# Kernel tuning notes

Measured on AMD Instinct MI355X. Metric: run time of the kernel, lower is better.

## Reference

```python
import jax, jax.numpy as jnp
import numpy as np

N = 100000      # nodes
E = 3200000     # edges (before self-loops)
F_IN = 512      # input feature dim
H1, H2 = 64, 128
C = 40          # num classes
EPS = 1e-5      # BatchNorm eps


def setup_inputs() -> dict:
    key = jax.random.key(0)
    ks = jax.random.split(key, 20)
    inp = {
        "x": jax.random.normal(ks[0], (N, F_IN), jnp.float32),
        "edge_index": jax.random.randint(ks[1], (2, E), 0, N, dtype=jnp.int64),
        # GCNConv weights/biases (glorot-ish scale)
        "W1": jax.random.normal(ks[2], (F_IN, H1), jnp.float32) * (1.0 / np.sqrt(F_IN)),
        "b1": jnp.zeros((H1,), jnp.float32),
        "W2": jax.random.normal(ks[3], (H1, H2), jnp.float32) * (1.0 / np.sqrt(H1)),
        "b2": jnp.zeros((H2,), jnp.float32),
        "W3": jax.random.normal(ks[4], (H2, C), jnp.float32) * (1.0 / np.sqrt(H2)),
        "b3": jnp.zeros((C,), jnp.float32),
        # BatchNorm (eval mode: running stats)
        "g1": 1.0 + 0.1 * jax.random.normal(ks[5], (H1,), jnp.float32),
        "bt1": 0.1 * jax.random.normal(ks[6], (H1,), jnp.float32),
        "rm1": 0.1 * jax.random.normal(ks[7], (H1,), jnp.float32),
        "rv1": jax.random.uniform(ks[8], (H1,), jnp.float32, 0.5, 1.5),
        "g2": 1.0 + 0.1 * jax.random.normal(ks[9], (H2,), jnp.float32),
        "bt2": 0.1 * jax.random.normal(ks[10], (H2,), jnp.float32),
        "rm2": 0.1 * jax.random.normal(ks[11], (H2,), jnp.float32),
        "rv2": jax.random.uniform(ks[12], (H2,), jnp.float32, 0.5, 1.5),
    }
    return inp


def _gcn_norm(edge_index):
    # add self-loops, compute sym-normalized edge weights: d^-1/2[src]*d^-1/2[dst]
    loop = jnp.arange(N, dtype=edge_index.dtype)
    src = jnp.concatenate([edge_index[0], loop])
    dst = jnp.concatenate([edge_index[1], loop])
    deg = jax.ops.segment_sum(jnp.ones_like(dst, jnp.float32), dst, num_segments=N)
    dinv = 1.0 / jnp.sqrt(deg)  # deg >= 1 thanks to self-loops
    norm = dinv[src] * dinv[dst]  # [E+N]
    return src, dst, norm


def _gcn_conv(x, W, b, src, dst, norm):
    h = x @ W                                   # [N, out]
    msg = h[src] * norm[:, None]                # [E+N, out] gather + per-edge scale
    agg = jax.ops.segment_sum(msg, dst, num_segments=N)  # scatter-add
    return agg + b


def _bn_eval(x, gamma, beta, mean, var):
    return (x - mean) * (gamma / jnp.sqrt(var + EPS)) + beta


def reference(x, edge_index, W1, b1, W2, b2, W3, b3,
              g1, bt1, rm1, rv1, g2, bt2, rm2, rv2):
    src, dst, norm = _gcn_norm(edge_index)
    h = jax.nn.relu(_bn_eval(_gcn_conv(x, W1, b1, src, dst, norm), g1, bt1, rm1, rv1))
    # dropout p=0.3: identity in eval mode
    h = jax.nn.relu(_bn_eval(_gcn_conv(h, W2, b2, src, dst, norm), g2, bt2, rm2, rv2))
    h = _gcn_conv(h, W3, b3, src, dst, norm)
    return jax.nn.log_softmax(h, axis=1)
```

## Files before the change

### kernel.cpp

```cpp
#include <hip/hip_runtime.h>
#include <hip/hip_bf16.h>

#define NN 100000
#define FIN 512
#define H1D 64
#define H2D 128
#define CD 40
#define GP 64
#define BNEPS 1e-5f

#define BSHIFT 9
#define BSZ 512
#define NB 196
#define CHUNK 8192

typedef __attribute__((ext_vector_type(8))) short bf16x8;
typedef __attribute__((ext_vector_type(4))) float f32x4;

__device__ __forceinline__ float bf2f(ushort u) {
    union { uint i; float f; } v; v.i = ((uint)u) << 16; return v.f;
}
__device__ __forceinline__ ushort f2bf(float f) {
    union { float f; uint i; } v; v.f = f;
    uint x = v.i;
    return (ushort)((x + 0x7fffu + ((x >> 16) & 1u)) >> 16);
}

__device__ __forceinline__ void acc8(float* a, uint4 v) {
    a[0] += bf2f((ushort)(v.x & 0xffff)); a[1] += bf2f((ushort)(v.x >> 16));
    a[2] += bf2f((ushort)(v.y & 0xffff)); a[3] += bf2f((ushort)(v.y >> 16));
    a[4] += bf2f((ushort)(v.z & 0xffff)); a[5] += bf2f((ushort)(v.z >> 16));
    a[6] += bf2f((ushort)(v.w & 0xffff)); a[7] += bf2f((ushort)(v.w >> 16));
}

__device__ __forceinline__ uint4 selz(bool q, uint4 v) {
    return q ? v : make_uint4(0u, 0u, 0u, 0u);
}


__global__ __launch_bounds__(256) void bhist_k(const int* __restrict__ dst, int E,
                                               int* __restrict__ bcount) {
    __shared__ int h[NB];
    for (int i = threadIdx.x; i < NB; i += 256) h[i] = 0;
    __syncthreads();
    int i = blockIdx.x * blockDim.x + threadIdx.x;
    int st = gridDim.x * blockDim.x;
    for (; i < E; i += st) atomicAdd(&h[dst[i] >> BSHIFT], 1);
    __syncthreads();
    for (int j = threadIdx.x; j < NB; j += 256)
        if (h[j]) atomicAdd(&bcount[j], h[j]);
}

__global__ __launch_bounds__(256) void bscan_k(const int* __restrict__ bcount,
                                               int* __restrict__ bstart,
                                               int* __restrict__ bcursor) {
    __shared__ int sh[NB];
    int tid = threadIdx.x;
    if (tid < NB) sh[tid] = bcount[tid];
    __syncthreads();
    for (int off = 1; off < NB; off <<= 1) {
        int v = (tid < NB && tid >= off) ? sh[tid - off] : 0;
        __syncthreads();
        if (tid < NB) sh[tid] += v;
        __syncthreads();
    }
    if (tid < NB) {
        int s = tid ? sh[tid - 1] : 0;
        bstart[tid] = s;
        bcursor[tid] = s;
    }
    if (tid == 0) bstart[NB] = sh[NB - 1];
}

__global__ __launch_bounds__(256) void bscatter_k(const int* __restrict__ src,
                                                  const int* __restrict__ dst, int E,
                                                  int* __restrict__ bcursor,
                                                  int* __restrict__ ebuf) {
    __shared__ int hist[NB];
    __shared__ int loff[NB];
    __shared__ int lcur[NB];
    __shared__ int gbase[NB];
    __shared__ int sbuf[CHUNK];
    int tid = threadIdx.x;
    int e0 = blockIdx.x * CHUNK;
    int e1 = e0 + CHUNK; if (e1 > E) e1 = E;

    for (int i = tid; i < NB; i += 256) hist[i] = 0;
    __syncthreads();
    for (int i = e0 + tid; i < e1; i += 256) atomicAdd(&hist[dst[i] >> BSHIFT], 1);
    __syncthreads();
    int v = (tid < NB) ? hist[tid] : 0;
    __syncthreads();
    if (tid < NB) loff[tid] = v;
    __syncthreads();
    for (int off = 1; off < NB; off <<= 1) {
        int u = (tid < NB && tid >= off) ? loff[tid - off] : 0;
        __syncthreads();
        if (tid < NB) loff[tid] += u;
        __syncthreads();
    }
    if (tid < NB) {
        int excl = loff[tid] - v;
        loff[tid] = excl;
        lcur[tid] = excl;
        gbase[tid] = (v > 0) ? atomicAdd(&bcursor[tid], v) : 0;
    }
    __syncthreads();
    for (int i = e0 + tid; i < e1; i += 256) {
        int d = dst[i];
        int b = d >> BSHIFT;
        int pos = atomicAdd(&lcur[b], 1);
        sbuf[pos] = (src[i] << BSHIFT) | (d & (BSZ - 1));
    }
    __syncthreads();
    int wave = tid >> 6, lane = tid & 63;
    for (int b = wave; b < NB; b += 4) {
        int cnt = (b + 1 < NB ? loff[b + 1] : (e1 - e0)) - loff[b];
        int s0 = loff[b], d0 = gbase[b];
        for (int k = lane; k < cnt; k += 64) ebuf[d0 + k] = sbuf[s0 + k];
    }
}

__global__ __launch_bounds__(256) void bcsr_k(const int* __restrict__ ebuf,
                                              const int* __restrict__ bstart,
                                              int* __restrict__ rowstart,
                                              float* __restrict__ dinv,
                                              int* __restrict__ csr, int E) {
    __shared__ int ldeg[BSZ];
    __shared__ int lcur[BSZ];
    __shared__ int s2[256];
    int b = blockIdx.x, tid = threadIdx.x;
    int node0 = b << BSHIFT;
    int es = bstart[b], ee = bstart[b + 1];
    ldeg[tid] = 0; ldeg[tid + 256] = 0;
    __syncthreads();
    for (int i = es + tid; i < ee; i += 256) atomicAdd(&ldeg[ebuf[i] & (BSZ - 1)], 1);
    __syncthreads();
    int a0 = ldeg[2 * tid], a1 = ldeg[2 * tid + 1];
    s2[tid] = a0 + a1;
    __syncthreads();
    for (int off = 1; off < 256; off <<= 1) {
        int u = (tid >= off) ? s2[tid - off] : 0;
        __syncthreads();
        s2[tid] += u;
        __syncthreads();
    }
    int base2 = tid ? s2[tid - 1] : 0;
    int ex0 = base2, ex1 = base2 + a0;
    int n0 = node0 + 2 * tid, n1 = n0 + 1;
    if (n0 < NN) { rowstart[n0] = es + ex0; dinv[n0] = rsqrtf((float)(a0 + 1)); }
    if (n1 < NN) { rowstart[n1] = es + ex1; dinv[n1] = rsqrtf((float)(a1 + 1)); }
    lcur[2 * tid] = es + ex0;
    lcur[2 * tid + 1] = es + ex1;
    __syncthreads();
    for (int i = es + tid; i < ee; i += 256) {
        int e = ebuf[i];
        int pos = atomicAdd(&lcur[e & (BSZ - 1)], 1);
        csr[pos] = ((unsigned)e) >> BSHIFT;
    }
    if (b == 0 && tid == 0) rowstart[NN] = E;
}

__global__ __launch_bounds__(256) void w1cvt_k(const float* __restrict__ W1,
                                               ushort* __restrict__ w1t) {
    int i = blockIdx.x * 256 + threadIdx.x;
    if (i < FIN * H1D) {
        int n = i >> 9, k = i & 511;
        w1t[i] = f2bf(W1[k * H1D + n]);
    }
}

#define BPAD 520
__global__ __launch_bounds__(256) void gemm1_k(const float* __restrict__ x,
                                               const ushort* __restrict__ w1t,
                                               const float* __restrict__ dinv,
                                               ushort* __restrict__ t1) {
    __shared__ ushort sB[H1D * BPAD];
    int tid = threadIdx.x;
    {
        int row = tid >> 2, seg = tid & 3;
        const uint4* srcp = (const uint4*)(w1t + row * FIN + seg * 128);
        uint4* dstp = (uint4*)(sB + row * BPAD + seg * 128);
#pragma unroll
        for (int j = 0; j < 16; ++j) dstp[j] = srcp[j];
    }
    __syncthreads();
    int wave = tid >> 6, lane = tid & 63;
    int lm = lane & 15, q = lane >> 4;
    int r0 = blockIdx.x * 64 + wave * 16;
    int mrow = r0 + lm;
    int mc = mrow < NN ? mrow : NN - 1;
    const float* ap = x + (size_t)mc * FIN + q * 8;
    const ushort* bp = sB + (size_t)lm * BPAD + q * 8;
    f32x4 acc0 = {0.f, 0.f, 0.f, 0.f}, acc1 = acc0, acc2 = acc0, acc3 = acc0;
#pragma unroll 4
    for (int kb = 0; kb < FIN; kb += 32) {
        f32x4 a01 = __builtin_nontemporal_load((const f32x4*)(ap + kb));
        f32x4 a23 = __builtin_nontemporal_load((const f32x4*)(ap + kb + 4));
        union { bf16x8 v8; __hip_bfloat162 h2[4]; } ua;
        ua.h2[0] = __float22bfloat162_rn(make_float2(a01[0], a01[1]));
        ua.h2[1] = __float22bfloat162_rn(make_float2(a01[2], a01[3]));
        ua.h2[2] = __float22bfloat162_rn(make_float2(a23[0], a23[1]));
        ua.h2[3] = __float22bfloat162_rn(make_float2(a23[2], a23[3]));
        bf16x8 b0 = *(const bf16x8*)(bp + kb);
        bf16x8 b1 = *(const bf16x8*)(bp + 16 * BPAD + kb);
        bf16x8 b2 = *(const bf16x8*)(bp + 32 * BPAD + kb);
        bf16x8 b3 = *(const bf16x8*)(bp + 48 * BPAD + kb);
        acc0 = __builtin_amdgcn_mfma_f32_16x16x32_bf16(ua.v8, b0, acc0, 0, 0, 0);
        acc1 = __builtin_amdgcn_mfma_f32_16x16x32_bf16(ua.v8, b1, acc1, 0, 0, 0);
        acc2 = __builtin_amdgcn_mfma_f32_16x16x32_bf16(ua.v8, b2, acc2, 0, 0, 0);
        acc3 = __builtin_amdgcn_mfma_f32_16x16x32_bf16(ua.v8, b3, acc3, 0, 0, 0);
    }
    int rbase = r0 + q * 4;
#pragma unroll
    for (int r = 0; r < 4; ++r) {
        int row = rbase + r;
        if (row < NN) {
            float dv = dinv[row];
            ushort* o = t1 + (size_t)row * H1D;
            o[lm]      = f2bf(acc0[r] * dv);
            o[16 + lm] = f2bf(acc1[r] * dv);
            o[32 + lm] = f2bf(acc2[r] * dv);
            o[48 + lm] = f2bf(acc3[r] * dv);
        }
    }
}

template <int MODE>
__global__ __launch_bounds__(256) void agg64_k(const ushort* __restrict__ tin,
                                               ushort* __restrict__ tout,
                                               const int* __restrict__ rowstart,
                                               const int* __restrict__ csr,
                                               const float* __restrict__ dinv,
                                               const float* __restrict__ g,
                                               const float* __restrict__ bt,
                                               const float* __restrict__ rm,
                                               const float* __restrict__ rv,
                                               const float* __restrict__ b,
                                               int E) {
    int w = (blockIdx.x * blockDim.x + threadIdx.x) >> 6;
    int lane = threadIdx.x & 63;
    int nA = 2 * w;
    if (nA >= NN) return;
    int nB = nA + 1;
    int gsl = lane >> 3, c = lane & 7;
    int base = 8 * c;
    int2 r01 = *(const int2*)(rowstart + nA);
    int reB = rowstart[nA + 2];
    int iA = r01.x, reA = r01.y;
    int iB = reA;
    int Em1 = E - 1;
    float a[8], y[8];
#pragma unroll
    for (int j = 0; j < 8; ++j) { a[j] = 0.f; y[j] = 0.f; }

    for (;;) {
        bool dA = (iA + 32 <= reA);
        bool dB = (iB + 32 <= reB);
        if (!(dA | dB)) break;
        int jA0 = dA ? iA + gsl      : Em1;
        int jA1 = dA ? iA + 8 + gsl  : Em1;
        int jA2 = dA ? iA + 16 + gsl : Em1;
        int jA3 = dA ? iA + 24 + gsl : Em1;
        int jB0 = dB ? iB + gsl      : Em1;
        int jB1 = dB ? iB + 8 + gsl  : Em1;
        int jB2 = dB ? iB + 16 + gsl : Em1;
        int jB3 = dB ? iB + 24 + gsl : Em1;
        int sA0 = csr[jA0], sA1 = csr[jA1], sA2 = csr[jA2], sA3 = csr[jA3];
        int sB0 = csr[jB0], sB1 = csr[jB1], sB2 = csr[jB2], sB3 = csr[jB3];
        uint4 vA0 = *(const uint4*)(tin + (size_t)sA0 * H1D + base);
        uint4 vA1 = *(const uint4*)(tin + (size_t)sA1 * H1D + base);
        uint4 vA2 = *(const uint4*)(tin + (size_t)sA2 * H1D + base);
        uint4 vA3 = *(const uint4*)(tin + (size_t)sA3 * H1D + base);
        uint4 vB0 = *(const uint4*)(tin + (size_t)sB0 * H1D + base);
        uint4 vB1 = *(const uint4*)(tin + (size_t)sB1 * H1D + base);
        uint4 vB2 = *(const uint4*)(tin + (size_t)sB2 * H1D + base);
        uint4 vB3 = *(const uint4*)(tin + (size_t)sB3 * H1D + base);
        vA0 = selz(dA, vA0); vA1 = selz(dA, vA1); vA2 = selz(dA, vA2); vA3 = selz(dA, vA3);
        vB0 = selz(dB, vB0); vB1 = selz(dB, vB1); vB2 = selz(dB, vB2); vB3 = selz(dB, vB3);
        acc8(a, vA0); acc8(a, vA1); acc8(a, vA2); acc8(a, vA3);
        acc8(y, vB0); acc8(y, vB1); acc8(y, vB2); acc8(y, vB3);
        iA += dA ? 32 : 0;
        iB += dB ? 32 : 0;
    }
    {
        bool qA0 = iA + gsl < reA,      qB0 = iB + gsl < reB;
        bool qA1 = iA + 8 + gsl < reA,  qB1 = iB + 8 + gsl < reB;
        bool qA2 = iA + 16 + gsl < reA, qB2 = iB + 16 + gsl < reB;
        bool qA3 = iA + 24 + gsl < reA, qB3 = iB + 24 + gsl < reB;
        int jA0 = qA0 ? iA + gsl      : Em1;
        int jA1 = qA1 ? iA + 8 + gsl  : Em1;
        int jA2 = qA2 ? iA + 16 + gsl : Em1;
        int jA3 = qA3 ? iA + 24 + gsl : Em1;
        int jB0 = qB0 ? iB + gsl      : Em1;
        int jB1 = qB1 ? iB + 8 + gsl  : Em1;
        int jB2 = qB2 ? iB + 16 + gsl : Em1;
        int jB3 = qB3 ? iB + 24 + gsl : Em1;
        int sA0 = csr[jA0], sA1 = csr[jA1], sA2 = csr[jA2], sA3 = csr[jA3];
        int sB0 = csr[jB0], sB1 = csr[jB1], sB2 = csr[jB2], sB3 = csr[jB3];
        uint4 vA0 = *(const uint4*)(tin + (size_t)sA0 * H1D + base);
        uint4 vA1 = *(const uint4*)(tin + (size_t)sA1 * H1D + base);
        uint4 vA2 = *(const uint4*)(tin + (size_t)sA2 * H1D + base);
        uint4 vA3 = *(const uint4*)(tin + (size_t)sA3 * H1D + base);
        uint4 vB0 = *(const uint4*)(tin + (size_t)sB0 * H1D + base);
        uint4 vB1 = *(const uint4*)(tin + (size_t)sB1 * H1D + base);
        uint4 vB2 = *(const uint4*)(tin + (size_t)sB2 * H1D + base);
        uint4 vB3 = *(const uint4*)(tin + (size_t)sB3 * H1D + base);
        vA0 = selz(qA0, vA0); vA1 = selz(qA1, vA1); vA2 = selz(qA2, vA2); vA3 = selz(qA3, vA3);
        vB0 = selz(qB0, vB0); vB1 = selz(qB1, vB1); vB2 = selz(qB2, vB2); vB3 = selz(qB3, vB3);
        acc8(a, vA0); acc8(a, vA1); acc8(a, vA2); acc8(a, vA3);
        acc8(y, vB0); acc8(y, vB1); acc8(y, vB2); acc8(y, vB3);
    }
    uint4 svA = *(const uint4*)(tin + (size_t)nA * H1D + base);
    uint4 svB = *(const uint4*)(tin + (size_t)nB * H1D + base);
#pragma unroll
    for (int j = 0; j < 8; ++j) a[j] += __shfl_xor(a[j], 8);
#pragma unroll
    for (int j = 0; j < 8; ++j) a[j] += __shfl_xor(a[j], 16);
#pragma unroll
    for (int j = 0; j < 8; ++j) a[j] += __shfl_xor(a[j], 32);
#pragma unroll
    for (int j = 0; j < 8; ++j) y[j] += __shfl_xor(y[j], 8);
#pragma unroll
    for (int j = 0; j < 8; ++j) y[j] += __shfl_xor(y[j], 16);
#pragma unroll
    for (int j = 0; j < 8; ++j) y[j] += __shfl_xor(y[j], 32);
    acc8(a, svA);
    acc8(y, svB);
    float2 dv2 = *(const float2*)(dinv + nA);
    float dv = (gsl == 0) ? dv2.x : dv2.y;
    float s[8];
#pragma unroll
    for (int j = 0; j < 8; ++j) s[j] = (gsl == 0) ? a[j] : y[j];
    float z[8];
    if (MODE == 1) {
        int f0 = base;
        float4 G0 = *(const float4*)(g + f0),  G1 = *(const float4*)(g + f0 + 4);
        float4 V0 = *(const float4*)(rv + f0), V1 = *(const float4*)(rv + f0 + 4);
        float4 B0 = *(const float4*)(b + f0),  B1 = *(const float4*)(b + f0 + 4);
        float4 M0 = *(const float4*)(rm + f0), M1 = *(const float4*)(rm + f0 + 4);
        float4 T0 = *(const float4*)(bt + f0), T1 = *(const float4*)(bt + f0 + 4);
        float sc[8] = { G0.x * rsqrtf(V0.x + BNEPS), G0.y * rsqrtf(V0.y + BNEPS),
                        G0.z * rsqrtf(V0.z + BNEPS), G0.w * rsqrtf(V0.w + BNEPS),
                        G1.x * rsqrtf(V1.x + BNEPS), G1.y * rsqrtf(V1.y + BNEPS),
                        G1.z * rsqrtf(V1.z + BNEPS), G1.w * rsqrtf(V1.w + BNEPS) };
        float sh[8] = { (B0.x - M0.x) * sc[0] + T0.x, (B0.y - M0.y) * sc[1] + T0.y,
                        (B0.z - M0.z) * sc[2] + T0.z, (B0.w - M0.w) * sc[3] + T0.w,
                        (B1.x - M1.x) * sc[4] + T1.x, (B1.y - M1.y) * sc[5] + T1.y,
                        (B1.z - M1.z) * sc[6] + T1.z, (B1.w - M1.w) * sc[7] + T1.w };
#pragma unroll
        for (int j = 0; j < 8; ++j)
            z[j] = fmaxf(s[j] * dv * sc[j] + sh[j], 0.f) * dv;
    } else {
#pragma unroll
        for (int j = 0; j < 8; ++j) z[j] = s[j] * dv;
    }
    if (gsl < 2) {
        uint4 o;
        o.x = (uint)f2bf(z[0]) | ((uint)f2bf(z[1]) << 16);
        o.y = (uint)f2bf(z[2]) | ((uint)f2bf(z[3]) << 16);
        o.z = (uint)f2bf(z[4]) | ((uint)f2bf(z[5]) << 16);
        o.w = (uint)f2bf(z[6]) | ((uint)f2bf(z[7]) << 16);
        *(uint4*)(tout + (size_t)(nA + gsl) * H1D + base) = o;
    }
}

__global__ __launch_bounds__(256) void p2p3_k(const ushort* __restrict__ u2,
                                              const float* __restrict__ W2,
                                              const float* __restrict__ b2,
                                              const float* __restrict__ W3,
                                              const float* __restrict__ g2,
                                              const float* __restrict__ bt2,
                                              const float* __restrict__ rm2,
                                              const float* __restrict__ rv2,
                                              const float* __restrict__ dinv,
                                              ushort* __restrict__ g3) {
    __shared__ float sW2[H1D * H2D];
    __shared__ float sW3[H2D * CD];
    __shared__ float sc2[H2D], sh2[H2D];
    int tid = threadIdx.x;
    for (int i = tid; i < H1D * H2D; i += 256) sW2[i] = W2[i];
    for (int i = tid; i < H2D * CD; i += 256) sW3[i] = W3[i];
    if (tid < H2D) {
        float s = g2[tid] * rsqrtf(rv2[tid] + BNEPS);
        sc2[tid] = s;
        sh2[tid] = (b2[tid] - rm2[tid]) * s + bt2[tid];
    }
    __syncthreads();
    int node = blockIdx.x * 256 + tid;
    if (node >= NN) return;
    float u[H1D];
    const uint4* up = (const uint4*)(u2 + (size_t)node * H1D);
#pragma unroll
    for (int i = 0; i < 8; ++i) {
        uint4 v = up[i];
        u[8 * i + 0] = bf2f((ushort)(v.x & 0xffff)); u[8 * i + 1] = bf2f((ushort)(v.x >> 16));
        u[8 * i + 2] = bf2f((ushort)(v.y & 0xffff)); u[8 * i + 3] = bf2f((ushort)(v.y >> 16));
        u[8 * i + 4] = bf2f((ushort)(v.z & 0xffff)); u[8 * i + 5] = bf2f((ushort)(v.z >> 16));
        u[8 * i + 6] = bf2f((ushort)(v.w & 0xffff)); u[8 * i + 7] = bf2f((ushort)(v.w >> 16));
    }
    float gacc[CD];
#pragma unroll
    for (int c = 0; c < CD; ++c) gacc[c] = 0.f;
    for (int fc = 0; fc < H2D; fc += 32) {
        float a[32];
#pragma unroll
        for (int j = 0; j < 32; ++j) a[j] = 0.f;
        for (int l = 0; l < H1D; ++l) {
            float ul = u[l];
            const float4* wr = (const float4*)&sW2[l * H2D + fc];
#pragma unroll
            for (int j = 0; j < 8; ++j) {
                float4 w = wr[j];
                a[4 * j]     += ul * w.x;
                a[4 * j + 1] += ul * w.y;
                a[4 * j + 2] += ul * w.z;
                a[4 * j + 3] += ul * w.w;
            }
        }
#pragma unroll
        for (int j = 0; j < 32; ++j) {
            int f = fc + j;
            float hv = fmaxf(a[j] * sc2[f] + sh2[f], 0.f);
            const float4* w3r = (const float4*)&sW3[f * CD];
#pragma unroll
            for (int c = 0; c < 10; ++c) {
                float4 w = w3r[c];
                gacc[4 * c]     += hv * w.x;
                gacc[4 * c + 1] += hv * w.y;
                gacc[4 * c + 2] += hv * w.z;
                gacc[4 * c + 3] += hv * w.w;
            }
        }
    }
    float dv = dinv[node];
    ushort* op = g3 + (size_t)node * GP;
#pragma unroll
    for (int c = 0; c < 10; ++c) {
        uint pk  = (uint)f2bf(gacc[4 * c] * dv)     | ((uint)f2bf(gacc[4 * c + 1] * dv) << 16);
        uint pk2 = (uint)f2bf(gacc[4 * c + 2] * dv) | ((uint)f2bf(gacc[4 * c + 3] * dv) << 16);
        *(uint2*)&op[4 * c] = make_uint2(pk, pk2);
    }
}

__global__ __launch_bounds__(256) void agg40_k(const ushort* __restrict__ g3,
                                               const float* __restrict__ b3,
                                               const int* __restrict__ rowstart,
                                               const int* __restrict__ csr,
                                               const float* __restrict__ dinv,
                                               float* __restrict__ out,
                                               int E) {
    int w = (blockIdx.x * blockDim.x + threadIdx.x) >> 6;
    int lane = threadIdx.x & 63;
    int nA = 2 * w;
    if (nA >= NN) return;
    int nB = nA + 1;
    int gsl = lane >> 3, c = lane & 7;
    int base = 8 * c;
    int2 r01 = *(const int2*)(rowstart + nA);
    int reB = rowstart[nA + 2];
    int iA = r01.x, reA = r01.y;
    int iB = reA;
    int Em1 = E - 1;
    float a[8], y[8];
#pragma unroll
    for (int j = 0; j < 8; ++j) { a[j] = 0.f; y[j] = 0.f; }

    for (;;) {
        bool dA = (iA + 32 <= reA);
        bool dB = (iB + 32 <= reB);
        if (!(dA | dB)) break;
        int jA0 = dA ? iA + gsl      : Em1;
        int jA1 = dA ? iA + 8 + gsl  : Em1;
        int jA2 = dA ? iA + 16 + gsl : Em1;
        int jA3 = dA ? iA + 24 + gsl : Em1;
        int jB0 = dB ? iB + gsl      : Em1;
        int jB1 = dB ? iB + 8 + gsl  : Em1;
        int jB2 = dB ? iB + 16 + gsl : Em1;
        int jB3 = dB ? iB + 24 + gsl : Em1;
        int sA0 = csr[jA0], sA1 = csr[jA1], sA2 = csr[jA2], sA3 = csr[jA3];
        int sB0 = csr[jB0], sB1 = csr[jB1], sB2 = csr[jB2], sB3 = csr[jB3];
        uint4 vA0 = *(const uint4*)(g3 + (size_t)sA0 * GP + base);
        uint4 vA1 = *(const uint4*)(g3 + (size_t)sA1 * GP + base);
        uint4 vA2 = *(const uint4*)(g3 + (size_t)sA2 * GP + base);
        uint4 vA3 = *(const uint4*)(g3 + (size_t)sA3 * GP + base);
        uint4 vB0 = *(const uint4*)(g3 + (size_t)sB0 * GP + base);
        uint4 vB1 = *(const uint4*)(g3 + (size_t)sB1 * GP + base);
        uint4 vB2 = *(const uint4*)(g3 + (size_t)sB2 * GP + base);
        uint4 vB3 = *(const uint4*)(g3 + (size_t)sB3 * GP + base);
        vA0 = selz(dA, vA0); vA1 = selz(dA, vA1); vA2 = selz(dA, vA2); vA3 = selz(dA, vA3);
        vB0 = selz(dB, vB0); vB1 = selz(dB, vB1); vB2 = selz(dB, vB2); vB3 = selz(dB, vB3);
        acc8(a, vA0); acc8(a, vA1); acc8(a, vA2); acc8(a, vA3);
        acc8(y, vB0); acc8(y, vB1); acc8(y, vB2); acc8(y, vB3);
        iA += dA ? 32 : 0;
        iB += dB ? 32 : 0;
    }
    {
        bool qA0 = iA + gsl < reA,      qB0 = iB + gsl < reB;
        bool qA1 = iA + 8 + gsl < reA,  qB1 = iB + 8 + gsl < reB;
        bool qA2 = iA + 16 + gsl < reA, qB2 = iB + 16 + gsl < reB;
        bool qA3 = iA + 24 + gsl < reA, qB3 = iB + 24 + gsl < reB;
        int jA0 = qA0 ? iA + gsl      : Em1;
        int jA1 = qA1 ? iA + 8 + gsl  : Em1;
        int jA2 = qA2 ? iA + 16 + gsl : Em1;
        int jA3 = qA3 ? iA + 24 + gsl : Em1;
        int jB0 = qB0 ? iB + gsl      : Em1;
        int jB1 = qB1 ? iB + 8 + gsl  : Em1;
        int jB2 = qB2 ? iB + 16 + gsl : Em1;
        int jB3 = qB3 ? iB + 24 + gsl : Em1;
        int sA0 = csr[jA0], sA1 = csr[jA1], sA2 = csr[jA2], sA3 = csr[jA3];
        int sB0 = csr[jB0], sB1 = csr[jB1], sB2 = csr[jB2], sB3 = csr[jB3];
        uint4 vA0 = *(const uint4*)(g3 + (size_t)sA0 * GP + base);
        uint4 vA1 = *(const uint4*)(g3 + (size_t)sA1 * GP + base);
        uint4 vA2 = *(const uint4*)(g3 + (size_t)sA2 * GP + base);
        uint4 vA3 = *(const uint4*)(g3 + (size_t)sA3 * GP + base);
        uint4 vB0 = *(const uint4*)(g3 + (size_t)sB0 * GP + base);
        uint4 vB1 = *(const uint4*)(g3 + (size_t)sB1 * GP + base);
        uint4 vB2 = *(const uint4*)(g3 + (size_t)sB2 * GP + base);
        uint4 vB3 = *(const uint4*)(g3 + (size_t)sB3 * GP + base);
        vA0 = selz(qA0, vA0); vA1 = selz(qA1, vA1); vA2 = selz(qA2, vA2); vA3 = selz(qA3, vA3);
        vB0 = selz(qB0, vB0); vB1 = selz(qB1, vB1); vB2 = selz(qB2, vB2); vB3 = selz(qB3, vB3);
        acc8(a, vA0); acc8(a, vA1); acc8(a, vA2); acc8(a, vA3);
        acc8(y, vB0); acc8(y, vB1); acc8(y, vB2); acc8(y, vB3);
    }
    uint4 svA = *(const uint4*)(g3 + (size_t)nA * GP + base);
    uint4 svB = *(const uint4*)(g3 + (size_t)nB * GP + base);
#pragma unroll
    for (int j = 0; j < 8; ++j) a[j] += __shfl_xor(a[j], 8);
#pragma unroll
    for (int j = 0; j < 8; ++j) a[j] += __shfl_xor(a[j], 16);
#pragma unroll
    for (int j = 0; j < 8; ++j) a[j] += __shfl_xor(a[j], 32);
#pragma unroll
    for (int j = 0; j < 8; ++j) y[j] += __shfl_xor(y[j], 8);
#pragma unroll
    for (int j = 0; j < 8; ++j) y[j] += __shfl_xor(y[j], 16);
#pragma unroll
    for (int j = 0; j < 8; ++j) y[j] += __shfl_xor(y[j], 32);
    acc8(a, svA);
    acc8(y, svB);
    float2 dv2 = *(const float2*)(dinv + nA);
    float dv = (gsl == 0) ? dv2.x : dv2.y;
    float s[8];
#pragma unroll
    for (int j = 0; j < 8; ++j) s[j] = (gsl == 0) ? a[j] : y[j];
    float z[8];
    if (c < 5) {
        float4 bb0 = *(const float4*)(b3 + base);
        float4 bb1 = *(const float4*)(b3 + base + 4);
        z[0] = s[0] * dv + bb0.x; z[1] = s[1] * dv + bb0.y;
        z[2] = s[2] * dv + bb0.z; z[3] = s[3] * dv + bb0.w;
        z[4] = s[4] * dv + bb1.x; z[5] = s[5] * dv + bb1.y;
        z[6] = s[6] * dv + bb1.z; z[7] = s[7] * dv + bb1.w;
    } else {
#pragma unroll
        for (int j = 0; j < 8; ++j) z[j] = -1e30f;
    }
    float m = fmaxf(fmaxf(fmaxf(z[0], z[1]), fmaxf(z[2], z[3])),
                    fmaxf(fmaxf(z[4], z[5]), fmaxf(z[6], z[7])));
    m = fmaxf(m, __shfl_xor(m, 1));
    m = fmaxf(m, __shfl_xor(m, 2));
    m = fmaxf(m, __shfl_xor(m, 4));
    float e = 0.f;
    if (c < 5) {
#pragma unroll
        for (int j = 0; j < 8; ++j) e += __expf(z[j] - m);
    }
    e += __shfl_xor(e, 1);
    e += __shfl_xor(e, 2);
    e += __shfl_xor(e, 4);
    float ls = __logf(e);
    if (gsl < 2 && c < 5) {
        float4 o0 = { z[0] - m - ls, z[1] - m - ls, z[2] - m - ls, z[3] - m - ls };
        float4 o1 = { z[4] - m - ls, z[5] - m - ls, z[6] - m - ls, z[7] - m - ls };
        float* orow = out + (size_t)(nA + gsl) * CD + base;
        *(float4*)(orow)     = o0;
        *(float4*)(orow + 4) = o1;
    }
}


extern "C" void kernel_launch(void* const* d_in, const int* in_sizes, int n_in,
                              void* d_out, int out_size, void* d_ws, size_t ws_size,
                              hipStream_t stream) {
    (void)n_in; (void)out_size; (void)ws_size;
    const float* x   = (const float*)d_in[0];
    const int*   ei  = (const int*)d_in[1];
    const float* W1  = (const float*)d_in[2];
    const float* b1  = (const float*)d_in[3];
    const float* W2  = (const float*)d_in[4];
    const float* b2  = (const float*)d_in[5];
    const float* W3  = (const float*)d_in[6];
    const float* b3  = (const float*)d_in[7];
    const float* g1  = (const float*)d_in[8];
    const float* bt1 = (const float*)d_in[9];
    const float* rm1 = (const float*)d_in[10];
    const float* rv1 = (const float*)d_in[11];
    const float* g2  = (const float*)d_in[12];
    const float* bt2 = (const float*)d_in[13];
    const float* rm2 = (const float*)d_in[14];
    const float* rv2 = (const float*)d_in[15];
    float* out = (float*)d_out;
    const int E = in_sizes[1] / 2;

    char* w = (char*)d_ws;
    auto alloc = [&](size_t bytes) { char* p = w; w += (bytes + 511) & ~(size_t)511; return p; };
    int*    bcount   = (int*)alloc((size_t)NB * 4);
    int*    bstart   = (int*)alloc((size_t)(NB + 1) * 4);
    int*    bcursor  = (int*)alloc((size_t)NB * 4);
    int*    rowstart = (int*)alloc((size_t)(NN + 1) * 4);
    float*  dinv     = (float*)alloc((size_t)NN * 4);
    int*    csr      = (int*)alloc((size_t)E * 4);
    int*    ebuf     = (int*)alloc((size_t)E * 4);
    ushort* w1t      = (ushort*)alloc((size_t)H1D * FIN * 2);
    ushort* t1       = (ushort*)alloc((size_t)NN * H1D * 2);
    ushort* t2       = (ushort*)alloc((size_t)NN * H1D * 2);
    ushort* g3       = (ushort*)alloc((size_t)NN * GP * 2);

    const int aggblocks = ((NN / 2) + 3) / 4;

    hipMemsetAsync(bcount, 0, (size_t)NB * 4, stream);
    bhist_k<<<512, 256, 0, stream>>>(ei + E, E, bcount);
    bscan_k<<<1, 256, 0, stream>>>(bcount, bstart, bcursor);
    bscatter_k<<<(E + CHUNK - 1) / CHUNK, 256, 0, stream>>>(ei, ei + E, E, bcursor, ebuf);
    bcsr_k<<<NB, 256, 0, stream>>>(ebuf, bstart, rowstart, dinv, csr, E);
    w1cvt_k<<<(FIN * H1D + 255) / 256, 256, 0, stream>>>(W1, w1t);
    gemm1_k<<<(NN + 63) / 64, 256, 0, stream>>>(x, w1t, dinv, t1);
    agg64_k<1><<<aggblocks, 256, 0, stream>>>(t1, t2, rowstart, csr, dinv, g1, bt1, rm1, rv1, b1, E);
    agg64_k<2><<<aggblocks, 256, 0, stream>>>(t2, t1, rowstart, csr, dinv, nullptr, nullptr, nullptr, nullptr, nullptr, E);
    p2p3_k<<<(NN + 255) / 256, 256, 0, stream>>>(t1, W2, b2, W3, g2, bt2, rm2, rv2, dinv, g3);
    agg40_k<<<aggblocks, 256, 0, stream>>>(g3, b3, rowstart, csr, dinv, out, E);
}
```

Before: 714.0 us.

## Fuse second aggregation with W2/W3 projection; enlarge gemm1 blocks to 512 threads

Replaces the separate layer-2 aggregation kernel and per-node dense projection kernel with one kernel. It aggregates neighbours per wave, stages the aggregated rows in shared memory, then does the W2 (bf16-packed) and W3 (transposed) matvecs cooperatively across lanes. This removes a full intermediate write and read of the N×64 tensor and one launch. It also replaces the register-heavy per-thread matvec, at the cost of bf16 rounding of W2. Separately, gemm1 now uses 512-thread blocks covering 128 rows each, so the W1 tile staged in shared memory is shared by twice as many rows.

After: 756.2 us. 5.9% more time.

```diff
diff --git a/kernel.cpp b/kernel.cpp
--- a/kernel.cpp
+++ b/kernel.cpp
@@ -171,23 +171,23 @@
 }
 
 #define BPAD 520
-__global__ __launch_bounds__(256) void gemm1_k(const float* __restrict__ x,
+__global__ __launch_bounds__(512) void gemm1_k(const float* __restrict__ x,
                                                const ushort* __restrict__ w1t,
                                                const float* __restrict__ dinv,
                                                ushort* __restrict__ t1) {
     __shared__ ushort sB[H1D * BPAD];
     int tid = threadIdx.x;
     {
-        int row = tid >> 2, seg = tid & 3;
-        const uint4* srcp = (const uint4*)(w1t + row * FIN + seg * 128);
-        uint4* dstp = (uint4*)(sB + row * BPAD + seg * 128);
-#pragma unroll
-        for (int j = 0; j < 16; ++j) dstp[j] = srcp[j];
+        int row = tid >> 3, seg = tid & 7;
+        const uint4* srcp = (const uint4*)(w1t + row * FIN + seg * 64);
+        uint4* dstp = (uint4*)(sB + row * BPAD + seg * 64);
+#pragma unroll
+        for (int j = 0; j < 8; ++j) dstp[j] = srcp[j];
     }
     __syncthreads();
     int wave = tid >> 6, lane = tid & 63;
     int lm = lane & 15, q = lane >> 4;
-    int r0 = blockIdx.x * 64 + wave * 16;
+    int r0 = blockIdx.x * 128 + wave * 16;
     int mrow = r0 + lm;
     int mc = mrow < NN ? mrow : NN - 1;
     const float* ap = x + (size_t)mc * FIN + q * 8;
@@ -365,7 +365,8 @@
     }
 }
 
-__global__ __launch_bounds__(256) void p2p3_k(const ushort* __restrict__ u2,
+#define APB 8
+__global__ __launch_bounds__(256) void aggp_k(const ushort* __restrict__ tin,
                                               const float* __restrict__ W2,
                                               const float* __restrict__ b2,
                                               const float* __restrict__ W3,
@@ -373,73 +374,168 @@
                                               const float* __restrict__ bt2,
                                               const float* __restrict__ rm2,
                                               const float* __restrict__ rv2,
+                                              const int* __restrict__ rowstart,
+                                              const int* __restrict__ csr,
                                               const float* __restrict__ dinv,
-                                              ushort* __restrict__ g3) {
-    __shared__ float sW2[H1D * H2D];
-    __shared__ float sW3[H2D * CD];
+                                              ushort* __restrict__ g3,
+                                              int E) {
+    __shared__ uint  sW2p[H1D * 64];
+    __shared__ float sW3T[CD][132];
     __shared__ float sc2[H2D], sh2[H2D];
+    __shared__ float su[APB][H1D];
+    __shared__ float sh[APB][H2D];
     int tid = threadIdx.x;
-    for (int i = tid; i < H1D * H2D; i += 256) sW2[i] = W2[i];
-    for (int i = tid; i < H2D * CD; i += 256) sW3[i] = W3[i];
+    for (int i = tid; i < H1D * 64; i += 256) {
+        int l = i >> 6, fl = i & 63;
+        uint pk = (uint)f2bf(W2[l * H2D + fl]) | ((uint)f2bf(W2[l * H2D + 64 + fl]) << 16);
+        sW2p[i] = pk;
+    }
+    for (int i = tid; i < H2D * CD; i += 256) {
+        int f = i / CD, o = i - f * CD;
+        sW3T[o][f] = W3[i];
+    }
     if (tid < H2D) {
         float s = g2[tid] * rsqrtf(rv2[tid] + BNEPS);
         sc2[tid] = s;
         sh2[tid] = (b2[tid] - rm2[tid]) * s + bt2[tid];
     }
     __syncthreads();
-    int node = blockIdx.x * 256 + tid;
-    if (node >= NN) return;
-    float u[H1D];
-    const uint4* up = (const uint4*)(u2 + (size_t)node * H1D);
-#pragma unroll
-    for (int i = 0; i < 8; ++i) {
-        uint4 v = up[i];
-        u[8 * i + 0] = bf2f((ushort)(v.x & 0xffff)); u[8 * i + 1] = bf2f((ushort)(v.x >> 16));
-        u[8 * i + 2] = bf2f((ushort)(v.y & 0xffff)); u[8 * i + 3] = bf2f((ushort)(v.y >> 16));
-        u[8 * i + 4] = bf2f((ushort)(v.z & 0xffff)); u[8 * i + 5] = bf2f((ushort)(v.z >> 16));
-        u[8 * i + 6] = bf2f((ushort)(v.w & 0xffff)); u[8 * i + 7] = bf2f((ushort)(v.w >> 16));
-    }
-    float gacc[CD];
-#pragma unroll
-    for (int c = 0; c < CD; ++c) gacc[c] = 0.f;
-    for (int fc = 0; fc < H2D; fc += 32) {
-        float a[32];
-#pragma unroll
-        for (int j = 0; j < 32; ++j) a[j] = 0.f;
-        for (int l = 0; l < H1D; ++l) {
-            float ul = u[l];
-            const float4* wr = (const float4*)&sW2[l * H2D + fc];
-#pragma unroll
-            for (int j = 0; j < 8; ++j) {
-                float4 w = wr[j];
-                a[4 * j]     += ul * w.x;
-                a[4 * j + 1] += ul * w.y;
-                a[4 * j + 2] += ul * w.z;
-                a[4 * j + 3] += ul * w.w;
-            }
+    int wave = tid >> 6, lane = tid & 63;
+    int nA = blockIdx.x * APB + 2 * wave;
+    if (nA >= NN) return;
+    int nB = nA + 1;
+    int gsl = lane >> 3, c = lane & 7;
+    int base = 8 * c;
+    int2 r01 = *(const int2*)(rowstart + nA);
+    int reB = rowstart[nA + 2];
+    int iA = r01.x, reA = r01.y;
+    int iB = reA;
+    int Em1 = E - 1;
+    float a[8], y[8];
+#pragma unroll
+    for (int j = 0; j < 8; ++j) { a[j] = 0.f; y[j] = 0.f; }
+
+    for (;;) {
+        bool dA = (iA + 32 <= reA);
+        bool dB = (iB + 32 <= reB);
+        if (!(dA | dB)) break;
+        int jA0 = dA ? iA + gsl      : Em1;
+        int jA1 = dA ? iA + 8 + gsl  : Em1;
+        int jA2 = dA ? iA + 16 + gsl : Em1;
+        int jA3 = dA ? iA + 24 + gsl : Em1;
+        int jB0 = dB ? iB + gsl      : Em1;
+        int jB1 = dB ? iB + 8 + gsl  : Em1;
+        int jB2 = dB ? iB + 16 + gsl : Em1;
+        int jB3 = dB ? iB + 24 + gsl : Em1;
+        int sA0 = csr[jA0], sA1 = csr[jA1], sA2 = csr[jA2], sA3 = csr[jA3];
+        int sB0 = csr[jB0], sB1 = csr[jB1], sB2 = csr[jB2], sB3 = csr[jB3];
+        uint4 vA0 = *(const uint4*)(tin + (size_t)sA0 * H1D + base);
+        uint4 vA1 = *(const uint4*)(tin + (size_t)sA1 * H1D + base);
+        uint4 vA2 = *(const uint4*)(tin + (size_t)sA2 * H1D + base);
+        uint4 vA3 = *(const uint4*)(tin + (size_t)sA3 * H1D + base);
+        uint4 vB0 = *(const uint4*)(tin + (size_t)sB0 * H1D + base);
+        uint4 vB1 = *(const uint4*)(tin + (size_t)sB1 * H1D + base);
+        uint4 vB2 = *(const uint4*)(tin + (size_t)sB2 * H1D + base);
+        uint4 vB3 = *(const uint4*)(tin + (size_t)sB3 * H1D + base);
+        vA0 = selz(dA, vA0); vA1 = selz(dA, vA1); vA2 = selz(dA, vA2); vA3 = selz(dA, vA3);
+        vB0 = selz(dB, vB0); vB1 = selz(dB, vB1); vB2 = selz(dB, vB2); vB3 = selz(dB, vB3);
+        acc8(a, vA0); acc8(a, vA1); acc8(a, vA2); acc8(a, vA3);
+        acc8(y, vB0); acc8(y, vB1); acc8(y, vB2); acc8(y, vB3);
+        iA += dA ? 32 : 0;
+        iB += dB ? 32 : 0;
+    }
+    {
+        bool qA0 = iA + gsl < reA,      qB0 = iB + gsl < reB;
+        bool qA1 = iA + 8 + gsl < reA,  qB1 = iB + 8 + gsl < reB;
+        bool qA2 = iA + 16 + gsl < reA, qB2 = iB + 16 + gsl < reB;
+        bool qA3 = iA + 24 + gsl < reA, qB3 = iB + 24 + gsl < reB;
+        int jA0 = qA0 ? iA + gsl      : Em1;
+        int jA1 = qA1 ? iA + 8 + gsl  : Em1;
+        int jA2 = qA2 ? iA + 16 + gsl : Em1;
+        int jA3 = qA3 ? iA + 24 + gsl : Em1;
+        int jB0 = qB0 ? iB + gsl      : Em1;
+        int jB1 = qB1 ? iB + 8 + gsl  : Em1;
+        int jB2 = qB2 ? iB + 16 + gsl : Em1;
+        int jB3 = qB3 ? iB + 24 + gsl : Em1;
+        int sA0 = csr[jA0], sA1 = csr[jA1], sA2 = csr[jA2], sA3 = csr[jA3];
+        int sB0 = csr[jB0], sB1 = csr[jB1], sB2 = csr[jB2], sB3 = csr[jB3];
+        uint4 vA0 = *(const uint4*)(tin + (size_t)sA0 * H1D + base);
+        uint4 vA1 = *(const uint4*)(tin + (size_t)sA1 * H1D + base);
+        uint4 vA2 = *(const uint4*)(tin + (size_t)sA2 * H1D + base);
+        uint4 vA3 = *(const uint4*)(tin + (size_t)sA3 * H1D + base);
+        uint4 vB0 = *(const uint4*)(tin + (size_t)sB0 * H1D + base);
+        uint4 vB1 = *(const uint4*)(tin + (size_t)sB1 * H1D + base);
+        uint4 vB2 = *(const uint4*)(tin + (size_t)sB2 * H1D + base);
+        uint4 vB3 = *(const uint4*)(tin + (size_t)sB3 * H1D + base);
+        vA0 = selz(qA0, vA0); vA1 = selz(qA1, vA1); vA2 = selz(qA2, vA2); vA3 = selz(qA3, vA3);
+        vB0 = selz(qB0, vB0); vB1 = selz(qB1, vB1); vB2 = selz(qB2, vB2); vB3 = selz(qB3, vB3);
+        acc8(a, vA0); acc8(a, vA1); acc8(a, vA2); acc8(a, vA3);
+        acc8(y, vB0); acc8(y, vB1); acc8(y, vB2); acc8(y, vB3);
+    }
+    uint4 svA = *(const uint4*)(tin + (size_t)nA * H1D + base);
+    uint4 svB = *(const uint4*)(tin + (size_t)nB * H1D + base);
+#pragma unroll
+    for (int j = 0; j < 8; ++j) a[j] += __shfl_xor(a[j], 8);
+#pragma unroll
+    for (int j = 0; j < 8; ++j) a[j] += __shfl_xor(a[j], 16);
+#pragma unroll
+    for (int j = 0; j < 8; ++j) a[j] += __shfl_xor(a[j], 32);
+#pragma unroll
+    for (int j = 0; j < 8; ++j) y[j] += __shfl_xor(y[j], 8);
+#pragma unroll
+    for (int j = 0; j < 8; ++j) y[j] += __shfl_xor(y[j], 16);
+#pragma unroll
+    for (int j = 0; j < 8; ++j) y[j] += __shfl_xor(y[j], 32);
+    acc8(a, svA);
+    acc8(y, svB);
+    float2 dv2 = *(const float2*)(dinv + nA);
+    if (gsl < 2) {
+        float dv = (gsl == 0) ? dv2.x : dv2.y;
+        int n = 2 * wave + gsl;
+        float s0 = (gsl == 0) ? a[0] : y[0], s1 = (gsl == 0) ? a[1] : y[1];
+        float s2v = (gsl == 0) ? a[2] : y[2], s3 = (gsl == 0) ? a[3] : y[3];
+        float s4 = (gsl == 0) ? a[4] : y[4], s5 = (gsl == 0) ? a[5] : y[5];
+        float s6 = (gsl == 0) ? a[6] : y[6], s7 = (gsl == 0) ? a[7] : y[7];
+        *(float4*)&su[n][base]     = make_float4(s0 * dv, s1 * dv, s2v * dv, s3 * dv);
+        *(float4*)&su[n][base + 4] = make_float4(s4 * dv, s5 * dv, s6 * dv, s7 * dv);
+    }
+    int n0 = 2 * wave, n1 = n0 + 1;
+    float hA0 = 0.f, hA1 = 0.f, hB0 = 0.f, hB1 = 0.f;
+#pragma unroll 4
+    for (int l4 = 0; l4 < H1D / 4; ++l4) {
+        float4 uA4 = *(const float4*)&su[n0][4 * l4];
+        float4 uB4 = *(const float4*)&su[n1][4 * l4];
+#pragma unroll
+        for (int k = 0; k < 4; ++k) {
+            uint w = sW2p[(4 * l4 + k) * 64 + lane];
+            float w0 = bf2f((ushort)(w & 0xffff));
+            float w1 = bf2f((ushort)(w >> 16));
+            float uA = (k == 0) ? uA4.x : (k == 1) ? uA4.y : (k == 2) ? uA4.z : uA4.w;
+            float uB = (k == 0) ? uB4.x : (k == 1) ? uB4.y : (k == 2) ? uB4.z : uB4.w;
+            hA0 += uA * w0; hA1 += uA * w1;
+            hB0 += uB * w0; hB1 += uB * w1;
         }
-#pragma unroll
-        for (int j = 0; j < 32; ++j) {
-            int f = fc + j;
-            float hv = fmaxf(a[j] * sc2[f] + sh2[f], 0.f);
-            const float4* w3r = (const float4*)&sW3[f * CD];
-#pragma unroll
-            for (int c = 0; c < 10; ++c) {
-                float4 w = w3r[c];
-                gacc[4 * c]     += hv * w.x;
-                gacc[4 * c + 1] += hv * w.y;
-                gacc[4 * c + 2] += hv * w.z;
-                gacc[4 * c + 3] += hv * w.w;
-            }
+    }
+    {
+        float c0 = sc2[lane], c1 = sc2[64 + lane];
+        float t0 = sh2[lane], t1v = sh2[64 + lane];
+        sh[n0][lane]      = fmaxf(hA0 * c0 + t0, 0.f);
+        sh[n0][64 + lane] = fmaxf(hA1 * c1 + t1v, 0.f);
+        sh[n1][lane]      = fmaxf(hB0 * c0 + t0, 0.f);
+        sh[n1][64 + lane] = fmaxf(hB1 * c1 + t1v, 0.f);
+    }
+    if (lane < CD) {
+        float gA = 0.f, gB = 0.f;
+#pragma unroll 4
+        for (int f4 = 0; f4 < H2D / 4; ++f4) {
+            float4 wv = *(const float4*)&sW3T[lane][4 * f4];
+            float4 ha = *(const float4*)&sh[n0][4 * f4];
+            float4 hb = *(const float4*)&sh[n1][4 * f4];
+            gA += wv.x * ha.x + wv.y * ha.y + wv.z * ha.z + wv.w * ha.w;
+            gB += wv.x * hb.x + wv.y * hb.y + wv.z * hb.z + wv.w * hb.w;
         }
-    }
-    float dv = dinv[node];
-    ushort* op = g3 + (size_t)node * GP;
-#pragma unroll
-    for (int c = 0; c < 10; ++c) {
-        uint pk  = (uint)f2bf(gacc[4 * c] * dv)     | ((uint)f2bf(gacc[4 * c + 1] * dv) << 16);
-        uint pk2 = (uint)f2bf(gacc[4 * c + 2] * dv) | ((uint)f2bf(gacc[4 * c + 3] * dv) << 16);
-        *(uint2*)&op[4 * c] = make_uint2(pk, pk2);
+        g3[(size_t)nA * GP + lane] = f2bf(gA * dv2.x);
+        g3[(size_t)nB * GP + lane] = f2bf(gB * dv2.y);
     }
 }
 
@@ -625,9 +721,8 @@
     bscatter_k<<<(E + CHUNK - 1) / CHUNK, 256, 0, stream>>>(ei, ei + E, E, bcursor, ebuf);
     bcsr_k<<<NB, 256, 0, stream>>>(ebuf, bstart, rowstart, dinv, csr, E);
     w1cvt_k<<<(FIN * H1D + 255) / 256, 256, 0, stream>>>(W1, w1t);
-    gemm1_k<<<(NN + 63) / 64, 256, 0, stream>>>(x, w1t, dinv, t1);
+    gemm1_k<<<(NN + 127) / 128, 512, 0, stream>>>(x, w1t, dinv, t1);
     agg64_k<1><<<aggblocks, 256, 0, stream>>>(t1, t2, rowstart, csr, dinv, g1, bt1, rm1, rv1, b1, E);
-    agg64_k<2><<<aggblocks, 256, 0, stream>>>(t2, t1, rowstart, csr, dinv, nullptr, nullptr, nullptr, nullptr, nullptr, E);
-    p2p3_k<<<(NN + 255) / 256, 256, 0, stream>>>(t1, W2, b2, W3, g2, bt2, rm2, rv2, dinv, g3);
+    aggp_k<<<NN / APB, 256, 0, stream>>>(t2, W2, b2, W3, g2, bt2, rm2, rv2, rowstart, csr, dinv, g3, E);
     agg40_k<<<aggblocks, 256, 0, stream>>>(g3, b3, rowstart, csr, dinv, out, E);
 }
```

## Move fused W2/W3 dense stage onto bf16 MFMA with split-precision weights

Applied to the files above, without the earlier changes.

Replaces the per-thread scalar FP32 W2→BN→ReLU→W3 kernel with a wave-level MFMA version. Weights are stored in LDS as hi/lo bf16 pairs to emulate near-FP32 accuracy, and the intermediate hidden tile is staged through per-wave shared memory. The grid is a fixed set of persistent-style blocks that each process several 16-row tiles. Separately, gemm1 moves to 512-thread blocks of 128 rows, which halves how many times W1 is loaded into LDS per row. The aim is to remove the heavy VALU/register-bound FMA loop, at the cost of extra MFMAs for precision compensation and more LDS traffic.

New measurement: 650.8 us. 8.8% less time.

```diff
diff --git a/kernel.cpp b/kernel.cpp
--- a/kernel.cpp
+++ b/kernel.cpp
@@ -171,23 +171,23 @@
 }
 
 #define BPAD 520
-__global__ __launch_bounds__(256) void gemm1_k(const float* __restrict__ x,
+__global__ __launch_bounds__(512) void gemm1_k(const float* __restrict__ x,
                                                const ushort* __restrict__ w1t,
                                                const float* __restrict__ dinv,
                                                ushort* __restrict__ t1) {
     __shared__ ushort sB[H1D * BPAD];
     int tid = threadIdx.x;
     {
-        int row = tid >> 2, seg = tid & 3;
-        const uint4* srcp = (const uint4*)(w1t + row * FIN + seg * 128);
-        uint4* dstp = (uint4*)(sB + row * BPAD + seg * 128);
-#pragma unroll
-        for (int j = 0; j < 16; ++j) dstp[j] = srcp[j];
+        int row = tid >> 3, seg = tid & 7;
+        const uint4* srcp = (const uint4*)(w1t + row * FIN + seg * 64);
+        uint4* dstp = (uint4*)(sB + row * BPAD + seg * 64);
+#pragma unroll
+        for (int j = 0; j < 8; ++j) dstp[j] = srcp[j];
     }
     __syncthreads();
     int wave = tid >> 6, lane = tid & 63;
     int lm = lane & 15, q = lane >> 4;
-    int r0 = blockIdx.x * 64 + wave * 16;
+    int r0 = blockIdx.x * 128 + wave * 16;
     int mrow = r0 + lm;
     int mc = mrow < NN ? mrow : NN - 1;
     const float* ap = x + (size_t)mc * FIN + q * 8;
@@ -365,81 +365,125 @@
     }
 }
 
-__global__ __launch_bounds__(256) void p2p3_k(const ushort* __restrict__ u2,
-                                              const float* __restrict__ W2,
-                                              const float* __restrict__ b2,
-                                              const float* __restrict__ W3,
-                                              const float* __restrict__ g2,
-                                              const float* __restrict__ bt2,
-                                              const float* __restrict__ rm2,
-                                              const float* __restrict__ rv2,
-                                              const float* __restrict__ dinv,
-                                              ushort* __restrict__ g3) {
-    __shared__ float sW2[H1D * H2D];
-    __shared__ float sW3[H2D * CD];
+#define W2S 66
+#define W3S 130
+#define HS  132
+__global__ __launch_bounds__(256) void p2p3m_k(const ushort* __restrict__ u2,
+                                               const float* __restrict__ W2,
+                                               const float* __restrict__ b2,
+                                               const float* __restrict__ W3,
+                                               const float* __restrict__ g2,
+                                               const float* __restrict__ bt2,
+                                               const float* __restrict__ rm2,
+                                               const float* __restrict__ rv2,
+                                               const float* __restrict__ dinv,
+                                               ushort* __restrict__ g3) {
+    __shared__ uint sW2p[H2D * W2S];
+    __shared__ uint sW3p[48 * W3S];
     __shared__ float sc2[H2D], sh2[H2D];
+    __shared__ float hbuf[4][16 * HS];
     int tid = threadIdx.x;
-    for (int i = tid; i < H1D * H2D; i += 256) sW2[i] = W2[i];
-    for (int i = tid; i < H2D * CD; i += 256) sW3[i] = W3[i];
+    for (int i = tid; i < H1D * H2D; i += 256) {
+        int k = i >> 7, col = i & 127;
+        float wv = W2[i];
+        ushort hi = f2bf(wv);
+        ushort lo = f2bf(wv - bf2f(hi));
+        sW2p[col * W2S + k] = (uint)hi | ((uint)lo << 16);
+    }
+    for (int i = tid; i < 8 * H2D; i += 256)
+        sW3p[(40 + (i >> 7)) * W3S + (i & 127)] = 0u;
+    for (int i = tid; i < H2D * CD; i += 256) {
+        int k = i / CD, o = i - k * CD;
+        float wv = W3[i];
+        ushort hi = f2bf(wv);
+        ushort lo = f2bf(wv - bf2f(hi));
+        sW3p[o * W3S + k] = (uint)hi | ((uint)lo << 16);
+    }
     if (tid < H2D) {
         float s = g2[tid] * rsqrtf(rv2[tid] + BNEPS);
         sc2[tid] = s;
         sh2[tid] = (b2[tid] - rm2[tid]) * s + bt2[tid];
     }
     __syncthreads();
-    int node = blockIdx.x * 256 + tid;
-    if (node >= NN) return;
-    float u[H1D];
-    const uint4* up = (const uint4*)(u2 + (size_t)node * H1D);
-#pragma unroll
-    for (int i = 0; i < 8; ++i) {
-        uint4 v = up[i];
-        u[8 * i + 0] = bf2f((ushort)(v.x & 0xffff)); u[8 * i + 1] = bf2f((ushort)(v.x >> 16));
-        u[8 * i + 2] = bf2f((ushort)(v.y & 0xffff)); u[8 * i + 3] = bf2f((ushort)(v.y >> 16));
-        u[8 * i + 4] = bf2f((ushort)(v.z & 0xffff)); u[8 * i + 5] = bf2f((ushort)(v.z >> 16));
-        u[8 * i + 6] = bf2f((ushort)(v.w & 0xffff)); u[8 * i + 7] = bf2f((ushort)(v.w >> 16));
-    }
-    float gacc[CD];
-#pragma unroll
-    for (int c = 0; c < CD; ++c) gacc[c] = 0.f;
-    for (int fc = 0; fc < H2D; fc += 32) {
-        float a[32];
-#pragma unroll
-        for (int j = 0; j < 32; ++j) a[j] = 0.f;
-        for (int l = 0; l < H1D; ++l) {
-            float ul = u[l];
-            const float4* wr = (const float4*)&sW2[l * H2D + fc];
-#pragma unroll
-            for (int j = 0; j < 8; ++j) {
-                float4 w = wr[j];
-                a[4 * j]     += ul * w.x;
-                a[4 * j + 1] += ul * w.y;
-                a[4 * j + 2] += ul * w.z;
-                a[4 * j + 3] += ul * w.w;
+    int wave = tid >> 6, lane = tid & 63;
+    int lm = lane & 15, q = lane >> 4;
+    float* hb = hbuf[wave];
+    for (int t = 0; t < 7; ++t) {
+        int tile = blockIdx.x * 28 + wave * 7 + t;
+        int r0 = tile * 16;
+        if (r0 >= NN) break;
+        int mrow = r0 + lm;
+        int mc = mrow < NN ? mrow : NN - 1;
+        bf16x8 a0 = *(const bf16x8*)(u2 + (size_t)mc * H1D + q * 8);
+        bf16x8 a1 = *(const bf16x8*)(u2 + (size_t)mc * H1D + 32 + q * 8);
+#pragma unroll
+        for (int cb = 0; cb < 8; ++cb) {
+            int col = cb * 16 + lm;
+            const uint* wp = sW2p + col * W2S + q * 8;
+            f32x4 acc = {0.f, 0.f, 0.f, 0.f};
+#pragma unroll
+            for (int kb = 0; kb < 2; ++kb) {
+                const uint* w = wp + kb * 32;
+                union { bf16x8 v; uint u[4]; } bh, bl;
+#pragma unroll
+                for (int p = 0; p < 4; ++p) {
+                    uint w0 = w[2 * p], w1 = w[2 * p + 1];
+                    bh.u[p] = (w0 & 0xffffu) | (w1 << 16);
+                    bl.u[p] = (w0 >> 16) | (w1 & 0xffff0000u);
+                }
+                bf16x8 av = (kb == 0) ? a0 : a1;
+                acc = __builtin_amdgcn_mfma_f32_16x16x32_bf16(av, bh.v, acc, 0, 0, 0);
+                acc = __builtin_amdgcn_mfma_f32_16x16x32_bf16(av, bl.v, acc, 0, 0, 0);
+            }
+            float scv = sc2[col], shv = sh2[col];
+#pragma unroll
+            for (int r = 0; r < 4; ++r)
+                hb[(q * 4 + r) * HS + col] = fmaxf(acc[r] * scv + shv, 0.f);
+        }
+        f32x4 g0 = {0.f, 0.f, 0.f, 0.f}, g1v = g0, g2v = g0;
+#pragma unroll
+        for (int kb = 0; kb < 4; ++kb) {
+            const float* hp = hb + lm * HS + kb * 32 + q * 8;
+            union { bf16x8 v; uint u[4]; } ah, al;
+#pragma unroll
+            for (int p = 0; p < 2; ++p) {
+                float4 h4 = *(const float4*)(hp + 4 * p);
+                ushort h0 = f2bf(h4.x), h1 = f2bf(h4.y), h2 = f2bf(h4.z), h3 = f2bf(h4.w);
+                ah.u[2 * p]     = (uint)h0 | ((uint)h1 << 16);
+                ah.u[2 * p + 1] = (uint)h2 | ((uint)h3 << 16);
+                ushort l0 = f2bf(h4.x - bf2f(h0)), l1 = f2bf(h4.y - bf2f(h1));
+                ushort l2 = f2bf(h4.z - bf2f(h2)), l3 = f2bf(h4.w - bf2f(h3));
+                al.u[2 * p]     = (uint)l0 | ((uint)l1 << 16);
+                al.u[2 * p + 1] = (uint)l2 | ((uint)l3 << 16);
+            }
+#pragma unroll
+            for (int cb = 0; cb < 3; ++cb) {
+                const uint* w = sW3p + (cb * 16 + lm) * W3S + kb * 32 + q * 8;
+                union { bf16x8 v; uint u[4]; } bh, bl;
+#pragma unroll
+                for (int p = 0; p < 4; ++p) {
+                    uint w0 = w[2 * p], w1 = w[2 * p + 1];
+                    bh.u[p] = (w0 & 0xffffu) | (w1 << 16);
+                    bl.u[p] = (w0 >> 16) | (w1 & 0xffff0000u);
+                }
+                f32x4 acc = (cb == 0) ? g0 : (cb == 1) ? g1v : g2v;
+                acc = __builtin_amdgcn_mfma_f32_16x16x32_bf16(ah.v, bh.v, acc, 0, 0, 0);
+                acc = __builtin_amdgcn_mfma_f32_16x16x32_bf16(ah.v, bl.v, acc, 0, 0, 0);
+                acc = __builtin_amdgcn_mfma_f32_16x16x32_bf16(al.v, bh.v, acc, 0, 0, 0);
+                if (cb == 0) g0 = acc; else if (cb == 1) g1v = acc; else g2v = acc;
             }
         }
 #pragma unroll
-        for (int j = 0; j < 32; ++j) {
-            int f = fc + j;
-            float hv = fmaxf(a[j] * sc2[f] + sh2[f], 0.f);
-            const float4* w3r = (const float4*)&sW3[f * CD];
-#pragma unroll
-            for (int c = 0; c < 10; ++c) {
-                float4 w = w3r[c];
-                gacc[4 * c]     += hv * w.x;
-                gacc[4 * c + 1] += hv * w.y;
-                gacc[4 * c + 2] += hv * w.z;
-                gacc[4 * c + 3] += hv * w.w;
+        for (int r = 0; r < 4; ++r) {
+            int row = r0 + q * 4 + r;
+            if (row < NN) {
+                float dv = dinv[row];
+                ushort* op = g3 + (size_t)row * GP;
+                op[lm]      = f2bf(g0[r] * dv);
+                op[16 + lm] = f2bf(g1v[r] * dv);
+                if (lm < 8) op[32 + lm] = f2bf(g2v[r] * dv);
             }
         }
-    }
-    float dv = dinv[node];
-    ushort* op = g3 + (size_t)node * GP;
-#pragma unroll
-    for (int c = 0; c < 10; ++c) {
-        uint pk  = (uint)f2bf(gacc[4 * c] * dv)     | ((uint)f2bf(gacc[4 * c + 1] * dv) << 16);
-        uint pk2 = (uint)f2bf(gacc[4 * c + 2] * dv) | ((uint)f2bf(gacc[4 * c + 3] * dv) << 16);
-        *(uint2*)&op[4 * c] = make_uint2(pk, pk2);
     }
 }
 
@@ -625,9 +669,9 @@
     bscatter_k<<<(E + CHUNK - 1) / CHUNK, 256, 0, stream>>>(ei, ei + E, E, bcursor, ebuf);
     bcsr_k<<<NB, 256, 0, stream>>>(ebuf, bstart, rowstart, dinv, csr, E);
     w1cvt_k<<<(FIN * H1D + 255) / 256, 256, 0, stream>>>(W1, w1t);
-    gemm1_k<<<(NN + 63) / 64, 256, 0, stream>>>(x, w1t, dinv, t1);
+    gemm1_k<<<(NN + 127) / 128, 512, 0, stream>>>(x, w1t, dinv, t1);
     agg64_k<1><<<aggblocks, 256, 0, stream>>>(t1, t2, rowstart, csr, dinv, g1, bt1, rm1, rv1, b1, E);
     agg64_k<2><<<aggblocks, 256, 0, stream>>>(t2, t1, rowstart, csr, dinv, nullptr, nullptr, nullptr, nullptr, nullptr, E);
-    p2p3_k<<<(NN + 255) / 256, 256, 0, stream>>>(t1, W2, b2, W3, g2, bt2, rm2, rv2, dinv, g3);
+    p2p3m_k<<<224, 256, 0, stream>>>(t1, W2, b2, W3, g2, bt2, rm2, rv2, dinv, g3);
     agg40_k<<<aggblocks, 256, 0, stream>>>(g3, b3, rowstart, csr, dinv, out, E);
 }
```
